# Optimization experiments

Measured on AMD Instinct MI355X. Metric: run time of the kernel, lower is better.

Reference implementation:

```python
import jax, jax.numpy as jnp
import numpy as np

B, S, HID = 1, 2048, 2048
H, D = 16, 128          # num heads, head_dim (H*D == HID)
L = 32                  # compression / selection block size
NB = S // L             # number of key blocks
NSEL = 8                # top-n selected blocks per query
WIN = 512               # sliding window size
SCALE = 1.0 / np.sqrt(D)
NEG = -1e9


def rotate_half(x):
    x1, x2 = x[..., : x.shape[-1] // 2], x[..., x.shape[-1] // 2 :]
    return jnp.concatenate([-x2, x1], axis=-1)


def rope_tables(dim, end, theta=10000.0):
    freqs = 1.0 / theta ** (jnp.arange(0, dim, 2, dtype=jnp.float32) / dim)
    ang = jnp.outer(jnp.arange(end, dtype=jnp.float32), freqs)  # [end, dim/2]
    cos = jnp.concatenate([jnp.cos(ang), jnp.cos(ang)], axis=-1)  # [end, dim]
    sin = jnp.concatenate([jnp.sin(ang), jnp.sin(ang)], axis=-1)
    return cos, sin


def setup_inputs() -> dict:
    key = jax.random.key(0)
    ks = jax.random.split(key, 10)
    std = 0.02
    return {
        "hidden_states": jax.random.normal(ks[0], (B, S, HID), jnp.float32),
        "Wq": jax.random.normal(ks[1], (HID, H * D), jnp.float32) * std,
        "bq": jnp.zeros((H * D,), jnp.float32),
        "Wk": jax.random.normal(ks[2], (HID, H * D), jnp.float32) * std,
        "bk": jnp.zeros((H * D,), jnp.float32),
        "Wv": jax.random.normal(ks[3], (HID, H * D), jnp.float32) * std,
        "bv": jnp.zeros((H * D,), jnp.float32),
        "Wg": jax.random.normal(ks[4], (H, D, 3), jnp.float32) * std,
        "bg": jnp.zeros((3,), jnp.float32),
    }


def _nsa_forward(hidden_states, Wq, bq, Wk, bk, Wv, bv, Wg, bg):
    # projections -> [B, H, S, D]
    def proj(W, b):
        return (hidden_states @ W + b).reshape(B, S, H, D).transpose(0, 2, 1, 3)

    q, k, v = proj(Wq, bq), proj(Wk, bk), proj(Wv, bv)

    cos, sin = rope_tables(D, S)  # [S, D]
    cos, sin = cos[None, None], sin[None, None]
    q = q * cos + rotate_half(q) * sin
    k = k * cos + rotate_half(k) * sin

    i = jnp.arange(S)
    t = jnp.arange(S)
    causal = t[None, :] <= i[:, None]  # [S, S]

    # ---- compressed branch: block mean-pooled K/V ----
    k_cmp = k.reshape(B, H, NB, L, D).mean(axis=3)  # [B,H,NB,D]
    v_cmp = v.reshape(B, H, NB, L, D).mean(axis=3)
    # block j visible if it ends at or before query position i
    blk_ok = ((jnp.arange(NB) + 1) * L - 1)[None, :] <= i[:, None]  # [S, NB]
    s_cmp = jnp.einsum("bhid,bhjd->bhij", q, k_cmp) * SCALE  # [B,H,S,NB]
    p_cmp = jax.nn.softmax(jnp.where(blk_ok[None, None], s_cmp, NEG), axis=-1)
    has_blk = blk_ok.any(axis=-1).astype(q.dtype)[None, None, :, None]  # [1,1,S,1]
    out_cmp = jnp.einsum("bhij,bhjd->bhid", p_cmp, v_cmp) * has_blk

    # ---- selection branch: top-n blocks from compressed scores ----
    idx = jax.lax.top_k(p_cmp, NSEL)[1]  # [B,H,S,NSEL]
    block_sel = (idx[..., None] == jnp.arange(NB)).any(axis=-2)  # [B,H,S,NB]
    cur_blk = (i[:, None] // L) == jnp.arange(NB)[None, :]  # always include own block
    block_sel = block_sel | cur_blk[None, None]
    tok_sel = jnp.take(block_sel, t // L, axis=-1)  # [B,H,S,S]
    mask_sel = tok_sel & causal[None, None]

    s = jnp.einsum("bhid,bhjd->bhij", q, k) * SCALE
    p_sel = jax.nn.softmax(jnp.where(mask_sel, s, NEG), axis=-1)
    out_sel = jnp.einsum("bhij,bhjd->bhid", p_sel, v)

    # ---- sliding-window branch ----
    mask_win = causal & ((i[:, None] - t[None, :]) < WIN)
    p_win = jax.nn.softmax(jnp.where(mask_win[None, None], s, NEG), axis=-1)
    out_win = jnp.einsum("bhij,bhjd->bhid", p_win, v)

    # ---- gated combine ----
    g = jax.nn.sigmoid(jnp.einsum("bhsd,hdg->bhsg", q, Wg) + bg)  # [B,H,S,3]
    out = (g[..., 0:1] * out_cmp + g[..., 1:2] * out_sel + g[..., 2:3] * out_win)
    return out.transpose(0, 2, 1, 3).reshape(B, S, H * D)


def reference(hidden_states, Wq, bq, Wk, bk, Wv, bv, Wg, bg):
    return _nsa_forward(hidden_states, Wq, bq, Wk, bk, Wv, bv, Wg, bg)
```

## Files before the change

kernel.cpp:

```cpp
#include <hip/hip_runtime.h>


#define SCALE_F 0.08838834764831845f
#define SCL2E   (0.08838834764831845f * 1.4426950408889634f)

typedef short  bf16x8 __attribute__((ext_vector_type(8)));
typedef short  s16x4  __attribute__((ext_vector_type(4)));
typedef float  f32x4  __attribute__((ext_vector_type(4)));

__device__ __forceinline__ unsigned short f2bfu(float x){
    unsigned u = __builtin_bit_cast(unsigned, x);
    u = (u + 0x7FFFu + ((u >> 16) & 1u)) >> 16;
    return (unsigned short)u;
}
__device__ __forceinline__ float bf2f(unsigned short b){
    unsigned u = ((unsigned)b) << 16;
    return __builtin_bit_cast(float, u);
}
__device__ __forceinline__ f32x4 mfma16(bf16x8 a, bf16x8 b, f32x4 c){
    return __builtin_amdgcn_mfma_f32_16x16x32_bf16(a, b, c, 0, 0, 0);
}

__global__ __launch_bounds__(64) void rope_table_k(float* __restrict__ ct,
                                                   float* __restrict__ st){
    int s = blockIdx.x, j = threadIdx.x;
    float fr  = 1.0f / powf(10000.0f, (float)j * (1.0f / 64.0f));
    float ang = (float)s * fr;
    ct[s * 64 + j] = cosf(ang);
    st[s * 64 + j] = sinf(ang);
}

__global__ __launch_bounds__(256) void prep_split(const float* __restrict__ src,
                                                  unsigned short* __restrict__ hi,
                                                  unsigned short* __restrict__ lo){
    size_t i = ((size_t)blockIdx.x * 256 + threadIdx.x) * 4;
    float4 x = *(const float4*)&src[i];
    unsigned short h0 = f2bfu(x.x), h1 = f2bfu(x.y), h2 = f2bfu(x.z), h3 = f2bfu(x.w);
    s16x4 hv; hv[0] = (short)h0; hv[1] = (short)h1; hv[2] = (short)h2; hv[3] = (short)h3;
    *(s16x4*)&hi[i] = hv;
    s16x4 lv;
    lv[0] = (short)f2bfu(x.x - bf2f(h0)); lv[1] = (short)f2bfu(x.y - bf2f(h1));
    lv[2] = (short)f2bfu(x.z - bf2f(h2)); lv[3] = (short)f2bfu(x.w - bf2f(h3));
    *(s16x4*)&lo[i] = lv;
}

__global__ __launch_bounds__(256) void prep_wT(const float* __restrict__ W,
                                               unsigned short* __restrict__ Th,
                                               unsigned short* __restrict__ Tl){
    __shared__ float T[64][65];
    const int k0 = blockIdx.x * 64, n0 = blockIdx.y * 64;
    const int tid = (int)threadIdx.x;
    #pragma unroll
    for (int it = 0; it < 16; ++it){
        int idx = tid + it * 256;
        int r = idx >> 6, c = idx & 63;
        T[c][r] = W[(size_t)(k0 + r) * 2048 + n0 + c];
    }
    __syncthreads();
    #pragma unroll
    for (int it = 0; it < 16; ++it){
        int idx = tid + it * 256;
        int n = idx >> 6, k = idx & 63;
        float v = T[n][k];
        unsigned short h = f2bfu(v);
        Th[(size_t)(n0 + n) * 2048 + k0 + k] = h;
        if (Tl) Tl[(size_t)(n0 + n) * 2048 + k0 + k] = f2bfu(v - bf2f(h));
    }
}

template <int P>
__global__ __launch_bounds__(256) void gemm_bf(
    const unsigned short* __restrict__ Ah, const unsigned short* __restrict__ Al,
    const unsigned short* __restrict__ Bh, const unsigned short* __restrict__ Bl,
    const float* __restrict__ bias,
    float* __restrict__ outF, unsigned short* __restrict__ outT)
{
    const unsigned short* Ap[2] = {Ah, Al};
    const unsigned short* Bp[2] = {Bh, Bl};

    const int bid = (int)blockIdx.x;
    const int xcd = bid & 7, idx = bid >> 3;
    const int m0  = (((xcd >> 1) << 2) + (idx & 3)) * 128;
    const int h   = ((xcd & 1) << 3) + (idx >> 2);

    const int tid = (int)threadIdx.x;
    const int l   = tid & 63, w = tid >> 6;
    const int wr  = w >> 1,  wc = w & 1;
    const int cc  = l & 15,  g  = l >> 4;

    __shared__ short As[P][128][40];
    __shared__ short Bs[P][128][40];

    f32x4 acc[4][4] = {};
    bf16x8 ra[P][2], rb[P][2];

    auto LOADSTEP = [&](int k0){
        #pragma unroll
        for (int p = 0; p < P; ++p)
            #pragma unroll
            for (int it = 0; it < 2; ++it){
                int c = tid + it * 256;
                int row = c >> 2, col8 = (c & 3) * 8;
                ra[p][it] = *(const bf16x8*)&Ap[p][(size_t)(m0 + row) * 2048 + k0 + col8];
                rb[p][it] = *(const bf16x8*)&Bp[p][(size_t)(h * 128 + row) * 2048 + k0 + col8];
            }
    };
    auto STORESTEP = [&](){
        #pragma unroll
        for (int p = 0; p < P; ++p)
            #pragma unroll
            for (int it = 0; it < 2; ++it){
                int c = tid + it * 256;
                int row = c >> 2, col8 = (c & 3) * 8;
                *(bf16x8*)&As[p][row][col8] = ra[p][it];
                *(bf16x8*)&Bs[p][row][col8] = rb[p][it];
            }
    };

    LOADSTEP(0); STORESTEP(); __syncthreads();
    for (int k0 = 0; k0 < 2048; k0 += 32){
        bool more = (k0 + 32) < 2048;
        if (more) LOADSTEP(k0 + 32);

        bf16x8 ah[4], bh[4];
        #pragma unroll
        for (int mt = 0; mt < 4; ++mt)
            ah[mt] = *(const bf16x8*)&As[0][wr * 64 + mt * 16 + cc][g * 8];
        #pragma unroll
        for (int nt = 0; nt < 4; ++nt)
            bh[nt] = *(const bf16x8*)&Bs[0][wc * 64 + nt * 16 + cc][g * 8];
        if (P == 2){
            bf16x8 al[4], bl[4];
            #pragma unroll
            for (int mt = 0; mt < 4; ++mt)
                al[mt] = *(const bf16x8*)&As[P - 1][wr * 64 + mt * 16 + cc][g * 8];
            #pragma unroll
            for (int nt = 0; nt < 4; ++nt)
                bl[nt] = *(const bf16x8*)&Bs[P - 1][wc * 64 + nt * 16 + cc][g * 8];
            #pragma unroll
            for (int mt = 0; mt < 4; ++mt)
                #pragma unroll
                for (int nt = 0; nt < 4; ++nt){
                    acc[mt][nt] = mfma16(ah[mt], bh[nt], acc[mt][nt]);
                    acc[mt][nt] = mfma16(ah[mt], bl[nt], acc[mt][nt]);
                    acc[mt][nt] = mfma16(al[mt], bh[nt], acc[mt][nt]);
                }
        } else {
            #pragma unroll
            for (int mt = 0; mt < 4; ++mt)
                #pragma unroll
                for (int nt = 0; nt < 4; ++nt)
                    acc[mt][nt] = mfma16(ah[mt], bh[nt], acc[mt][nt]);
        }
        __syncthreads();
        if (more){ STORESTEP(); __syncthreads(); }
    }

    #pragma unroll
    for (int mt = 0; mt < 4; ++mt)
        #pragma unroll
        for (int nt = 0; nt < 4; ++nt)
            #pragma unroll
            for (int j = 0; j < 4; ++j){
                int srow = m0 + wr * 64 + mt * 16 + g * 4 + j;
                int col  = wc * 64 + nt * 16 + cc;
                float v = acc[mt][nt][j] + bias[h * 128 + col];
                if (outF) outF[((size_t)h * 2048 + srow) * 128 + col] = v;
                else      outT[((size_t)h * 128 + col) * 2048 + srow] = f2bfu(v);
            }
}

__global__ __launch_bounds__(256) void rope_apply(
    float* __restrict__ qf, float* __restrict__ kf,
    unsigned short* __restrict__ qbb, unsigned short* __restrict__ kbb,
    const float* __restrict__ ct, const float* __restrict__ st)
{
    int idx = blockIdx.x * 256 + (int)threadIdx.x;
    int j = idx & 63;
    int s = (idx >> 6) & 2047;
    int h = (idx >> 17) & 15;
    int a = idx >> 21;
    size_t off = ((size_t)h * 2048 + s) * 128;
    float* p = (a ? kf : qf) + off;
    unsigned short* pb = (a ? kbb : qbb) + off;
    float c = ct[s * 64 + j], sn = st[s * 64 + j];
    float x1 = p[j], x2 = p[j + 64];
    float y1 = x1 * c - x2 * sn;
    float y2 = x2 * c + x1 * sn;
    p[j]      = y1;  p[j + 64]  = y2;
    pb[j] = f2bfu(y1); pb[j + 64] = f2bfu(y2);
}

__global__ __launch_bounds__(256) void cmp_mean(
    const float* __restrict__ kf, const unsigned short* __restrict__ vtbf,
    float* __restrict__ kcmp, float* __restrict__ vcmp)
{
    int idx = blockIdx.x * 256 + (int)threadIdx.x;
    int d  = idx & 127;
    int nb = (idx >> 7) & 63;
    int h  = idx >> 13;
    const float* kp = &kf[((size_t)h * 2048 + nb * 32) * 128 + d];
    float sk = 0.f;
    #pragma unroll
    for (int t = 0; t < 32; ++t) sk += kp[t * 128];
    const unsigned short* vp = &vtbf[((size_t)h * 128 + d) * 2048 + nb * 32];
    float sv = 0.f;
    #pragma unroll
    for (int t = 0; t < 32; ++t) sv += bf2f(vp[t]);
    kcmp[((size_t)h * 64 + nb) * 128 + d] = sk * 0.03125f;
    vcmp[((size_t)h * 64 + nb) * 128 + d] = sv * 0.03125f;
}

__global__ __launch_bounds__(256) void cmp_attn(
    const float* __restrict__ qf, const float* __restrict__ kcmp,
    const float* __restrict__ vcmp,
    const float* __restrict__ Wg, const float* __restrict__ bg,
    float* __restrict__ out, float* __restrict__ gout,
    unsigned long long* __restrict__ bmask)
{
    const int h = blockIdx.y, qt = blockIdx.x, i0 = qt * 64;
    const int tid = (int)threadIdx.x;
    const int l = tid & 63, w = tid >> 6;
    const int ty = tid >> 4, tx = tid & 15;
    const int cc = l & 15, g = l >> 4;

    __shared__ __align__(16) char smem[65536];
    __shared__ float sgl[4][16][3];
    float4* qs4 = (float4*)smem;
    float4* kc4 = (float4*)(smem + 32768);
    unsigned short* vcT = (unsigned short*)smem;
    float* sc = (float*)(smem + 32768);
    unsigned short* ps = (unsigned short*)(smem + 32768 + 17408);

    #pragma unroll
    for (int it = 0; it < 8; ++it){
        int idx = tid + it * 256;
        int row = idx >> 5, c = idx & 31;
        int cs = c ^ ((row >> 2) & 7);
        qs4[row * 32 + cs] = *(const float4*)&qf[((size_t)h * 2048 + i0 + row) * 128 + c * 4];
        kc4[row * 32 + cs] = *(const float4*)&kcmp[((size_t)h * 64 + row) * 128 + c * 4];
    }
    __syncthreads();

    {
        int gi = l & 3, qq = l >> 2;
        if (gi < 3){
            int q = w * 16 + qq;
            float acc = 0.f;
            #pragma unroll
            for (int c = 0; c < 32; ++c){
                float4 qv = qs4[q * 32 + (c ^ ((q >> 2) & 7))];
                const float* wgp = &Wg[(size_t)h * 384 + (c * 4) * 3 + gi];
                acc += qv.x * wgp[0] + qv.y * wgp[3] + qv.z * wgp[6] + qv.w * wgp[9];
            }
            float gv = 1.f / (1.f + expf(-(acc + bg[gi])));
            sgl[w][qq][gi] = gv;
            gout[((size_t)h * 2048 + i0 + q) * 3 + gi] = gv;
        }
    }

    float acc[4][4] = {};
    #pragma unroll 2
    for (int k0 = 0; k0 < 32; ++k0){
        float4 qv[4], kv[4];
        #pragma unroll
        for (int j = 0; j < 4; ++j) qv[j] = qs4[(4 * ty + j) * 32 + (k0 ^ (ty & 7))];
        #pragma unroll
        for (int c = 0; c < 4; ++c) kv[c] = kc4[(4 * tx + c) * 32 + (k0 ^ (tx & 7))];
        #pragma unroll
        for (int j = 0; j < 4; ++j)
            #pragma unroll
            for (int c = 0; c < 4; ++c)
                acc[j][c] += qv[j].x * kv[c].x + qv[j].y * kv[c].y
                           + qv[j].z * kv[c].z + qv[j].w * kv[c].w;
    }
    __syncthreads();

    #pragma unroll
    for (int j = 0; j < 4; ++j){
        int r = 4 * ty + j, i = i0 + r;
        float4 sv;
        float* svp = (float*)&sv;
        #pragma unroll
        for (int c = 0; c < 4; ++c){
            int b = 4 * tx + c;
            svp[c] = (b * 32 + 31 <= i) ? acc[j][c] * SCALE_F : -1e9f;
        }
        *(float4*)&sc[r * 68 + 4 * tx] = sv;
    }
    #pragma unroll
    for (int it = 0; it < 8; ++it){
        int idx = tid + it * 256;
        int jb = idx >> 5, d4 = (idx & 31) * 4;
        float4 vx = *(const float4*)&vcmp[((size_t)h * 64 + jb) * 128 + d4];
        const float* vp = (const float*)&vx;
        #pragma unroll
        for (int jj = 0; jj < 4; ++jj)
            vcT[(d4 + jj) * 72 + jb] = f2bfu(vp[jj]);
    }
    __syncthreads();

    for (int qq = 0; qq < 16; ++qq){
        const int q = w * 16 + qq;
        float s = sc[q * 68 + l];
        float mx = s;
        #pragma unroll
        for (int off = 1; off < 64; off <<= 1) mx = fmaxf(mx, __shfl_xor(mx, off));
        float p = expf(s - mx);
        float sum = p;
        #pragma unroll
        for (int off = 1; off < 64; off <<= 1) sum += __shfl_xor(sum, off);
        p /= sum;
        ps[q * 72 + l] = f2bfu(p);

        unsigned long long sel = 1ULL << ((i0 + q) >> 5);
        unsigned long long key = (1ULL << 45) |
            ((unsigned long long)__builtin_bit_cast(unsigned, p) << 7) |
            (unsigned long long)(63 - l);
        #pragma unroll
        for (int it = 0; it < 8; ++it){
            unsigned long long k2 = key;
            #pragma unroll
            for (int off = 1; off < 64; off <<= 1){
                unsigned long long o = __shfl_xor(k2, off);
                k2 = (o > k2) ? o : k2;
            }
            int wb = 63 - (int)(k2 & 63ULL);
            sel |= 1ULL << wb;
            if (l == wb) key = 0ULL;
        }
        if (l == 0) bmask[(size_t)h * 2048 + i0 + q] = sel;
    }
    __syncthreads();

    f32x4 oacc[8] = {};
    #pragma unroll
    for (int kk = 0; kk < 2; ++kk){
        bf16x8 pa = *(const bf16x8*)&ps[(w * 16 + cc) * 72 + kk * 32 + g * 8];
        #pragma unroll
        for (int nt2 = 0; nt2 < 8; ++nt2){
            bf16x8 vfr = *(const bf16x8*)&vcT[(nt2 * 16 + cc) * 72 + kk * 32 + g * 8];
            oacc[nt2] = mfma16(pa, vfr, oacc[nt2]);
        }
    }
    #pragma unroll
    for (int j = 0; j < 4; ++j){
        int q = w * 16 + g * 4 + j, iq = i0 + q;
        float g0 = sgl[w][g * 4 + j][0];
        float f = (iq >= 31) ? g0 : 0.f;
        #pragma unroll
        for (int nt2 = 0; nt2 < 8; ++nt2)
            out[(size_t)iq * 2048 + h * 128 + nt2 * 16 + cc] = f * oacc[nt2][j];
    }
}

__global__ __launch_bounds__(256) void attn_fd(
    const unsigned short* __restrict__ qbf,
    const unsigned short* __restrict__ kbf,
    const unsigned short* __restrict__ vtbf,
    const unsigned long long* __restrict__ bmask,
    float* __restrict__ Osel, float* __restrict__ lsel,
    float* __restrict__ Owin, float* __restrict__ lwin)
{
    const int bx = (int)blockIdx.x;
    const int h  = bx & 15;
    const int rr = 79 - (bx >> 4);
    const int g4 = (rr >= 48) ? 3 : (rr >= 24) ? 2 : (rr >= 8) ? 1 : 0;
    const int r  = rr - 4 * g4 * (g4 + 1);
    const int qt = 8 * g4 + r / (g4 + 1);
    const int seg = r % (g4 + 1);
    const int nch = qt + 1, nseg = g4 + 1;
    const int chlo = seg * nch / nseg;
    const int chhi = (seg + 1) * nch / nseg;

    const int i0 = qt * 64;
    const int tid = (int)threadIdx.x;
    const int l = tid & 63, w = tid >> 6;
    const int cc = l & 15,  g = l >> 4;

    __shared__ short Ks[64][136];
    __shared__ short Vt[128][72];
    __shared__ short Ps[4][16][72];

    unsigned long long um = bmask[(size_t)h * 2048 + i0 + l];
    #pragma unroll
    for (int off = 1; off < 64; off <<= 1) um |= __shfl_xor(um, off);

    unsigned long long bm[4];
    int mrow[4];
    #pragma unroll
    for (int j = 0; j < 4; ++j){
        mrow[j] = i0 + w * 16 + g * 4 + j;
        bm[j] = bmask[(size_t)h * 2048 + mrow[j]];
    }

    bf16x8 qfrag[4];
    {
        const unsigned short* qrow = &qbf[((size_t)h * 2048 + i0 + w * 16 + cc) * 128];
        #pragma unroll
        for (int kk = 0; kk < 4; ++kk)
            qfrag[kk] = *(const bf16x8*)&qrow[kk * 32 + g * 8];
    }

    f32x4 oaccS[8] = {}, oaccW[8] = {};
    float lsumS[4] = {}, lsumW[4] = {};

    auto needed = [&](int ch)->bool {
        return (ch >= qt - 8) || (((um >> (2 * ch)) & 3ULL) != 0ULL);
    };

    bf16x8 rk[4], rv[4];
    auto LOADC = [&](int ch){
        #pragma unroll
        for (int it = 0; it < 4; ++it){
            int c = tid + it * 256;
            rk[it] = *(const bf16x8*)&kbf[((size_t)h * 2048 + ch * 64 + (c >> 4)) * 128 + (c & 15) * 8];
            rv[it] = *(const bf16x8*)&vtbf[((size_t)h * 128 + (c >> 3)) * 2048 + ch * 64 + (c & 7) * 8];
        }
    };
    auto STOREC = [&](){
        #pragma unroll
        for (int it = 0; it < 4; ++it){
            int c = tid + it * 256;
            *(bf16x8*)&Ks[c >> 4][(c & 15) * 8] = rk[it];
            *(bf16x8*)&Vt[c >> 3][(c & 7) * 8] = rv[it];
        }
    };

    int cur = chlo;
    while (cur < chhi && !needed(cur)) ++cur;
    if (cur < chhi){
        LOADC(cur); STOREC(); __syncthreads();

        while (cur < chhi){
            int nxt = cur + 1;
            while (nxt < chhi && !needed(nxt)) ++nxt;
            const bool more = (nxt < chhi);
            if (more) LOADC(nxt);

            f32x4 sacc[4] = {};
            #pragma unroll
            for (int kk = 0; kk < 4; ++kk)
                #pragma unroll
                for (int nt = 0; nt < 4; ++nt){
                    bf16x8 kfr = *(const bf16x8*)&Ks[nt * 16 + cc][kk * 32 + g * 8];
                    sacc[nt] = mfma16(qfrag[kk], kfr, sacc[nt]);
                }

            float pe[4][4];
            #pragma unroll
            for (int j = 0; j < 4; ++j)
                #pragma unroll
                for (int nt = 0; nt < 4; ++nt)
                    pe[j][nt] = exp2f(sacc[nt][j] * SCL2E);

            const int tbase = cur * 64;

            #pragma unroll
            for (int j = 0; j < 4; ++j){
                const int iq = mrow[j];
                const int row = g * 4 + j;
                float pacc = 0.f;
                #pragma unroll
                for (int nt = 0; nt < 4; ++nt){
                    int t = tbase + nt * 16 + cc;
                    bool o = (t <= iq) && (((bm[j] >> (t >> 5)) & 1ULL) != 0ULL);
                    float p = o ? pe[j][nt] : 0.f;
                    pacc += p;
                    Ps[w][row][nt * 16 + cc] = (short)f2bfu(p);
                }
                lsumS[j] += pacc;
            }
            #pragma unroll
            for (int kk = 0; kk < 2; ++kk){
                bf16x8 pa = *(const bf16x8*)&Ps[w][cc][kk * 32 + g * 8];
                #pragma unroll
                for (int nt2 = 0; nt2 < 8; ++nt2){
                    bf16x8 vfr = *(const bf16x8*)&Vt[nt2 * 16 + cc][kk * 32 + g * 8];
                    oaccS[nt2] = mfma16(pa, vfr, oaccS[nt2]);
                }
            }

            if (cur >= qt - 8){
                #pragma unroll
                for (int j = 0; j < 4; ++j){
                    const int iq = mrow[j];
                    const int row = g * 4 + j;
                    float pacc = 0.f;
                    #pragma unroll
                    for (int nt = 0; nt < 4; ++nt){
                        int t = tbase + nt * 16 + cc;
                        bool o = (t <= iq) && ((iq - t) < 512);
                        float p = o ? pe[j][nt] : 0.f;
                        pacc += p;
                        Ps[w][row][nt * 16 + cc] = (short)f2bfu(p);
                    }
                    lsumW[j] += pacc;
                }
                #pragma unroll
                for (int kk = 0; kk < 2; ++kk){
                    bf16x8 pa = *(const bf16x8*)&Ps[w][cc][kk * 32 + g * 8];
                    #pragma unroll
                    for (int nt2 = 0; nt2 < 8; ++nt2){
                        bf16x8 vfr = *(const bf16x8*)&Vt[nt2 * 16 + cc][kk * 32 + g * 8];
                        oaccW[nt2] = mfma16(pa, vfr, oaccW[nt2]);
                    }
                }
            }

            __syncthreads();
            if (more){ STOREC(); __syncthreads(); }
            cur = more ? nxt : chhi;
        }
    }

    #pragma unroll
    for (int j = 0; j < 4; ++j){
        const int iq = mrow[j];
        float ls = lsumS[j], lw = lsumW[j];
        #pragma unroll
        for (int off = 1; off < 16; off <<= 1){
            ls += __shfl_xor(ls, off);
            lw += __shfl_xor(lw, off);
        }
        if (cc == 0){
            atomicAdd(&lsel[(size_t)h * 2048 + iq], ls);
            atomicAdd(&lwin[(size_t)h * 2048 + iq], lw);
        }
        #pragma unroll
        for (int nt2 = 0; nt2 < 8; ++nt2){
            size_t po = ((size_t)h * 2048 + iq) * 128 + nt2 * 16 + cc;
            atomicAdd(&Osel[po], oaccS[nt2][j]);
            atomicAdd(&Owin[po], oaccW[nt2][j]);
        }
    }
}

__global__ __launch_bounds__(256) void finalize(
    const float* __restrict__ Osel, const float* __restrict__ lsel,
    const float* __restrict__ Owin, const float* __restrict__ lwin,
    const float* __restrict__ gates, float* __restrict__ out)
{
    int idx = blockIdx.x * 256 + (int)threadIdx.x;
    int d4 = (idx & 31) * 4;
    int s  = (idx >> 5) & 2047;
    int h  = idx >> 16;
    size_t hs = (size_t)h * 2048 + s;
    float g1 = gates[hs * 3 + 1], g2 = gates[hs * 3 + 2];
    float il = g1 / lsel[hs];
    float iw = g2 / lwin[hs];
    size_t po = hs * 128 + d4;
    float4 a = *(const float4*)&Osel[po];
    float4 b = *(const float4*)&Owin[po];
    float* op = &out[(size_t)s * 2048 + h * 128 + d4];
    float4 o = *(const float4*)op;
    o.x += a.x * il + b.x * iw;
    o.y += a.y * il + b.y * iw;
    o.z += a.z * il + b.z * iw;
    o.w += a.w * il + b.w * iw;
    *(float4*)op = o;
}

extern "C" void kernel_launch(void* const* d_in, const int* in_sizes, int n_in,
                              void* d_out, int out_size, void* d_ws, size_t ws_size,
                              hipStream_t stream)
{
    const float* X  = (const float*)d_in[0];
    const float* Wq = (const float*)d_in[1];
    const float* bq = (const float*)d_in[2];
    const float* Wk = (const float*)d_in[3];
    const float* bk = (const float*)d_in[4];
    const float* Wv = (const float*)d_in[5];
    const float* bv = (const float*)d_in[6];
    const float* Wg = (const float*)d_in[7];
    const float* bg = (const float*)d_in[8];
    float* out = (float*)d_out;

    const size_t MBs = (size_t)1 << 20;
    char* ws = (char*)d_ws;

    unsigned short* Xh  = (unsigned short*)(ws + 0 * MBs);
    unsigned short* Xl  = (unsigned short*)(ws + 8 * MBs);
    unsigned short* WTh = (unsigned short*)(ws + 16 * MBs);
    unsigned short* WTl = (unsigned short*)(ws + 24 * MBs);
    float* qf  = (float*)(ws + 32 * MBs);
    float* kf  = (float*)(ws + 48 * MBs);
    unsigned short* vtbf = (unsigned short*)(ws + 64 * MBs);
    unsigned short* qbf  = (unsigned short*)(ws + 16 * MBs);
    unsigned short* kbf  = (unsigned short*)(ws + 24 * MBs);
    float* Osel = (float*)(ws + 0 * MBs);
    float* Owin = (float*)(ws + 32 * MBs);
    const size_t SM = 72 * MBs;
    float* cost  = (float*)(ws + SM);
    float* sint  = (float*)(ws + SM + 524288);
    float* kcmp  = (float*)(ws + SM + 1048576);
    float* vcmp  = (float*)(ws + SM + 1572864);
    float* gatesb = (float*)(ws + SM + 2097152);
    unsigned long long* bmaskb = (unsigned long long*)(ws + SM + 2490368);
    float* lsel = (float*)(ws + SM + 2752512);
    float* lwin = (float*)(ws + SM + 2883584);

    rope_table_k<<<2048, 64, 0, stream>>>(cost, sint);
    prep_split<<<4096, 256, 0, stream>>>(X, Xh, Xl);

    prep_wT<<<dim3(32, 32), 256, 0, stream>>>(Wq, WTh, WTl);
    gemm_bf<2><<<256, 256, 0, stream>>>(Xh, Xl, WTh, WTl, bq, qf, nullptr);
    prep_wT<<<dim3(32, 32), 256, 0, stream>>>(Wk, WTh, WTl);
    gemm_bf<2><<<256, 256, 0, stream>>>(Xh, Xl, WTh, WTl, bk, kf, nullptr);
    prep_wT<<<dim3(32, 32), 256, 0, stream>>>(Wv, WTh, nullptr);
    gemm_bf<1><<<256, 256, 0, stream>>>(Xh, nullptr, WTh, nullptr, bv, nullptr, vtbf);

    rope_apply<<<16384, 256, 0, stream>>>(qf, kf, qbf, kbf, cost, sint);
    cmp_mean<<<512, 256, 0, stream>>>(kf, vtbf, kcmp, vcmp);
    cmp_attn<<<dim3(32, 16), 256, 0, stream>>>(qf, kcmp, vcmp, Wg, bg,
                                               out, gatesb, bmaskb);

    hipMemsetAsync(Osel, 0, 16 * MBs, stream);
    hipMemsetAsync(Owin, 0, 16 * MBs, stream);
    hipMemsetAsync(lsel, 0, 262144, stream);

    attn_fd<<<1280, 256, 0, stream>>>(qbf, kbf, vtbf, bmaskb,
                                      Osel, lsel, Owin, lwin);
    finalize<<<4096, 256, 0, stream>>>(Osel, lsel, Owin, lwin, gatesb, out);
}
```

Before: 591.7 us.

## Replace atomic split-KV output accumulation with bf16 per-segment partial buffers

Each attention split segment now writes its unnormalized selection and window outputs as bf16 partials into dedicated slots, instead of atomically adding fp32 values into shared output buffers. The finalize kernel sums the per-segment partials directly. This removes the two large output memsets and a high volume of global fp32 atomics. The selection P·V work is also skipped for key chunks whose blocks are not selected by any row. The trade-off is that rounding partials to bf16 before normalization adds precision error, and finalize does a few more scattered reads.

```diff
diff --git a/kernel.cpp b/kernel.cpp
--- a/kernel.cpp
+++ b/kernel.cpp
@@ -359,8 +359,9 @@
     const unsigned short* __restrict__ kbf,
     const unsigned short* __restrict__ vtbf,
     const unsigned long long* __restrict__ bmask,
-    float* __restrict__ Osel, float* __restrict__ lsel,
-    float* __restrict__ Owin, float* __restrict__ lwin)
+    unsigned short* __restrict__ Psel,
+    unsigned short* __restrict__ Pwin,
+    float* __restrict__ lsel, float* __restrict__ lwin)
 {
     const int bx = (int)blockIdx.x;
     const int h  = bx & 15;
@@ -456,28 +457,30 @@
 
             const int tbase = cur * 64;
 
-            #pragma unroll
-            for (int j = 0; j < 4; ++j){
-                const int iq = mrow[j];
-                const int row = g * 4 + j;
-                float pacc = 0.f;
-                #pragma unroll
-                for (int nt = 0; nt < 4; ++nt){
-                    int t = tbase + nt * 16 + cc;
-                    bool o = (t <= iq) && (((bm[j] >> (t >> 5)) & 1ULL) != 0ULL);
-                    float p = o ? pe[j][nt] : 0.f;
-                    pacc += p;
-                    Ps[w][row][nt * 16 + cc] = (short)f2bfu(p);
+            if (((um >> (2 * cur)) & 3ULL) != 0ULL){
+                #pragma unroll
+                for (int j = 0; j < 4; ++j){
+                    const int iq = mrow[j];
+                    const int row = g * 4 + j;
+                    float pacc = 0.f;
+                    #pragma unroll
+                    for (int nt = 0; nt < 4; ++nt){
+                        int t = tbase + nt * 16 + cc;
+                        bool o = (t <= iq) && (((bm[j] >> (t >> 5)) & 1ULL) != 0ULL);
+                        float p = o ? pe[j][nt] : 0.f;
+                        pacc += p;
+                        Ps[w][row][nt * 16 + cc] = (short)f2bfu(p);
+                    }
+                    lsumS[j] += pacc;
                 }
-                lsumS[j] += pacc;
-            }
-            #pragma unroll
-            for (int kk = 0; kk < 2; ++kk){
-                bf16x8 pa = *(const bf16x8*)&Ps[w][cc][kk * 32 + g * 8];
-                #pragma unroll
-                for (int nt2 = 0; nt2 < 8; ++nt2){
-                    bf16x8 vfr = *(const bf16x8*)&Vt[nt2 * 16 + cc][kk * 32 + g * 8];
-                    oaccS[nt2] = mfma16(pa, vfr, oaccS[nt2]);
+                #pragma unroll
+                for (int kk = 0; kk < 2; ++kk){
+                    bf16x8 pa = *(const bf16x8*)&Ps[w][cc][kk * 32 + g * 8];
+                    #pragma unroll
+                    for (int nt2 = 0; nt2 < 8; ++nt2){
+                        bf16x8 vfr = *(const bf16x8*)&Vt[nt2 * 16 + cc][kk * 32 + g * 8];
+                        oaccS[nt2] = mfma16(pa, vfr, oaccS[nt2]);
+                    }
                 }
             }
 
@@ -514,6 +517,28 @@
         }
     }
 
+    {
+        size_t sb = (((size_t)h * 80 + rr) * 64) * 128;
+        #pragma unroll
+        for (int j = 0; j < 4; ++j){
+            int row = w * 16 + g * 4 + j;
+            #pragma unroll
+            for (int nt2 = 0; nt2 < 8; ++nt2)
+                Psel[sb + (size_t)row * 128 + nt2 * 16 + cc] = f2bfu(oaccS[nt2][j]);
+        }
+    }
+    int wslot = (seg == nseg - 1) ? 1 : ((seg == nseg - 2) ? 0 : -1);
+    if (wslot >= 0){
+        int wunit = (qt < 8) ? qt : 8 + (qt - 8) * 2 + wslot;
+        size_t wb = (((size_t)h * 56 + wunit) * 64) * 128;
+        #pragma unroll
+        for (int j = 0; j < 4; ++j){
+            int row = w * 16 + g * 4 + j;
+            #pragma unroll
+            for (int nt2 = 0; nt2 < 8; ++nt2)
+                Pwin[wb + (size_t)row * 128 + nt2 * 16 + cc] = f2bfu(oaccW[nt2][j]);
+        }
+    }
     #pragma unroll
     for (int j = 0; j < 4; ++j){
         const int iq = mrow[j];
@@ -527,37 +552,51 @@
             atomicAdd(&lsel[(size_t)h * 2048 + iq], ls);
             atomicAdd(&lwin[(size_t)h * 2048 + iq], lw);
         }
-        #pragma unroll
-        for (int nt2 = 0; nt2 < 8; ++nt2){
-            size_t po = ((size_t)h * 2048 + iq) * 128 + nt2 * 16 + cc;
-            atomicAdd(&Osel[po], oaccS[nt2][j]);
-            atomicAdd(&Owin[po], oaccW[nt2][j]);
-        }
     }
 }
 
 __global__ __launch_bounds__(256) void finalize(
-    const float* __restrict__ Osel, const float* __restrict__ lsel,
-    const float* __restrict__ Owin, const float* __restrict__ lwin,
+    const unsigned short* __restrict__ Psel, const float* __restrict__ lsel,
+    const unsigned short* __restrict__ Pwin, const float* __restrict__ lwin,
     const float* __restrict__ gates, float* __restrict__ out)
 {
     int idx = blockIdx.x * 256 + (int)threadIdx.x;
     int d4 = (idx & 31) * 4;
     int s  = (idx >> 5) & 2047;
     int h  = idx >> 16;
+    int qt = s >> 6, row = s & 63;
+    int g4 = qt >> 3, nseg = g4 + 1;
+    int rr0 = 4 * g4 * (g4 + 1) + (qt - 8 * g4) * nseg;
+
+    float ax = 0.f, ay = 0.f, az = 0.f, aw = 0.f;
+    for (int sg = 0; sg < nseg; ++sg){
+        s16x4 v = *(const s16x4*)&Psel[(((size_t)h * 80 + rr0 + sg) * 64 + row) * 128 + d4];
+        ax += bf2f((unsigned short)v[0]); ay += bf2f((unsigned short)v[1]);
+        az += bf2f((unsigned short)v[2]); aw += bf2f((unsigned short)v[3]);
+    }
+    float bx = 0.f, by = 0.f, bz = 0.f, bw = 0.f;
+    {
+        int u1 = (qt < 8) ? qt : 8 + (qt - 8) * 2 + 1;
+        s16x4 v = *(const s16x4*)&Pwin[(((size_t)h * 56 + u1) * 64 + row) * 128 + d4];
+        bx = bf2f((unsigned short)v[0]); by = bf2f((unsigned short)v[1]);
+        bz = bf2f((unsigned short)v[2]); bw = bf2f((unsigned short)v[3]);
+        if (qt >= 8){
+            int u0 = 8 + (qt - 8) * 2;
+            s16x4 v0 = *(const s16x4*)&Pwin[(((size_t)h * 56 + u0) * 64 + row) * 128 + d4];
+            bx += bf2f((unsigned short)v0[0]); by += bf2f((unsigned short)v0[1]);
+            bz += bf2f((unsigned short)v0[2]); bw += bf2f((unsigned short)v0[3]);
+        }
+    }
     size_t hs = (size_t)h * 2048 + s;
     float g1 = gates[hs * 3 + 1], g2 = gates[hs * 3 + 2];
     float il = g1 / lsel[hs];
     float iw = g2 / lwin[hs];
-    size_t po = hs * 128 + d4;
-    float4 a = *(const float4*)&Osel[po];
-    float4 b = *(const float4*)&Owin[po];
     float* op = &out[(size_t)s * 2048 + h * 128 + d4];
     float4 o = *(const float4*)op;
-    o.x += a.x * il + b.x * iw;
-    o.y += a.y * il + b.y * iw;
-    o.z += a.z * il + b.z * iw;
-    o.w += a.w * il + b.w * iw;
+    o.x += ax * il + bx * iw;
+    o.y += ay * il + by * iw;
+    o.z += az * il + bz * iw;
+    o.w += aw * il + bw * iw;
     *(float4*)op = o;
 }
 
@@ -588,8 +627,8 @@
     unsigned short* vtbf = (unsigned short*)(ws + 64 * MBs);
     unsigned short* qbf  = (unsigned short*)(ws + 16 * MBs);
     unsigned short* kbf  = (unsigned short*)(ws + 24 * MBs);
-    float* Osel = (float*)(ws + 0 * MBs);
-    float* Owin = (float*)(ws + 32 * MBs);
+    unsigned short* PselB = (unsigned short*)(ws + 32 * MBs);
+    unsigned short* PwinB = (unsigned short*)(ws + 0 * MBs);
     const size_t SM = 72 * MBs;
     float* cost  = (float*)(ws + SM);
     float* sint  = (float*)(ws + SM + 524288);
@@ -615,11 +654,9 @@
     cmp_attn<<<dim3(32, 16), 256, 0, stream>>>(qf, kcmp, vcmp, Wg, bg,
                                                out, gatesb, bmaskb);
 
-    hipMemsetAsync(Osel, 0, 16 * MBs, stream);
-    hipMemsetAsync(Owin, 0, 16 * MBs, stream);
     hipMemsetAsync(lsel, 0, 262144, stream);
 
     attn_fd<<<1280, 256, 0, stream>>>(qbf, kbf, vtbf, bmaskb,
-                                      Osel, lsel, Owin, lwin);
-    finalize<<<4096, 256, 0, stream>>>(Osel, lsel, Owin, lwin, gatesb, out);
-}
+                                      PselB, PwinB, lsel, lwin);
+    finalize<<<4096, 256, 0, stream>>>(PselB, lsel, PwinB, lwin, gatesb, out);
+}
```

Result: faster. 558.8 us (-5.6%).
